# Kernel tuning notes

Hardware: AMD Instinct MI355X
Metric: run time of the kernel (lower is better)

## Reference

```python
import jax, jax.numpy as jnp
import numpy as np

B, L, D, G = 8, 4096, 1024, 128
EPS = 1e-5


def setup_inputs() -> dict:
    key = jax.random.key(0)
    k1, k2, k3 = jax.random.split(key, 3)
    x = jax.random.normal(k1, (B, L, D), dtype=jnp.float32)
    prev_count = jnp.ones((B,), dtype=jnp.int64)          # prior_count observations already seen
    prev_mean = jnp.zeros((B, G), dtype=jnp.float32)       # prior_mean expanded over batch
    prev_var = jnp.ones((B, G), dtype=jnp.float32)         # exp(prior_logv)=1 expanded over batch
    weight = 0.02 * jax.random.normal(k2, (D,), dtype=jnp.float32)  # gamma = weight + 1
    bias = 0.02 * jax.random.normal(k3, (D,), dtype=jnp.float32)
    padding_mask = jnp.ones((B, L), dtype=jnp.int32)       # 1 = valid token
    return {"x": x, "prev_count": prev_count, "prev_mean": prev_mean,
            "prev_var": prev_var, "weight": weight, "bias": bias,
            "padding_mask": padding_mask}


def reference(x, prev_count, prev_mean, prev_var, weight, bias, padding_mask):
    """Cumulative (online Welford / Chan) per-group timestep normalization.

    Running stats per (batch, group) are updated once per valid timestep by
    merging the d features of that group at that step; output normalizes each
    timestep with the stats *including* that step, then applies affine
    gamma = weight + 1, beta = bias. Padded steps leave stats unchanged.
    """
    Bs, Ls, Ds = x.shape
    Gs = prev_mean.shape[-1]
    d = Ds // Gs  # features per group
    gamma = (weight + 1.0).reshape(Gs, d)
    beta = bias.reshape(Gs, d)

    xg = x.reshape(Bs, Ls, Gs, d).transpose(1, 0, 2, 3)     # [L,B,G,d]
    mask = padding_mask.astype(x.dtype).T                   # [L,B]
    fd = jnp.asarray(d, x.dtype)

    def step(carry, inp):
        count, mean, var = carry        # [B], [B,G], [B,G]
        xt, mt = inp                    # [B,G,d], [B]
        mu = xt.mean(-1)                                    # per-step group mean [B,G]
        ssq = jnp.sum((xt - mu[..., None]) ** 2, -1)        # per-step group M2   [B,G]
        N = count * fd                                      # elements seen so far [B]
        Np = N + fd
        delta = mu - mean
        mean_n = mean + delta * (fd / Np)[:, None]
        M2_n = var * N[:, None] + ssq + (delta ** 2) * (N * fd / Np)[:, None]
        var_n = M2_n / Np[:, None]
        v = mt[:, None]                                     # 1 if valid else 0
        mean_u = mean + v * (mean_n - mean)
        var_u = var + v * (var_n - var)
        count_u = count + mt
        rstd = jax.lax.rsqrt(var_u + EPS)                   # cumrstd [B,G]
        y = (xt - mean_u[..., None]) * rstd[..., None] * gamma + beta
        return (count_u, mean_u, var_u), y

    count0 = prev_count.astype(x.dtype)
    (count_f, mean_f, var_f), ys = jax.lax.scan(
        step, (count0, prev_mean, prev_var), (xg, mask))
    y = ys.transpose(1, 0, 2, 3).reshape(Bs, Ls, Ds)
    return y, count_f.astype(jnp.int64), mean_f, var_f
```

## Files before the change

### kernel.cpp

```cpp
#include <hip/hip_runtime.h>

#define PB 8
#define PL 4096
#define PD 1024
#define PG 128
#define SEG 32
#define NSEG (PL / SEG)
#define NEPS 1e-5f

#define YSZ ((size_t)PB * PL * PD)
#define COUNT_OFF (YSZ)
#define MEAN_OFF (YSZ + PB)
#define VAR_OFF (YSZ + PB + (size_t)PB * PG)

typedef float vf4 __attribute__((ext_vector_type(4)));


__global__ __launch_bounds__(256) void k_agg(const float* __restrict__ x,
                                             const int* __restrict__ mask,
                                             float* __restrict__ aggN,
                                             float* __restrict__ aggS,
                                             float* __restrict__ aggQ) {
    int blk = blockIdx.x;
    int b = blk >> 7;
    int seg = blk & (NSEG - 1);
    int u = threadIdx.x;
    size_t row0 = (size_t)b * PL + (size_t)seg * SEG;
    const float4* xp = (const float4*)x + row0 * (PD / 4) + u;
    const int* mp = mask + b * PL + seg * SEG;

    float S = 0.f, Q = 0.f, Sb = 0.f, Qb = 0.f, nc = 0.f;
#pragma unroll 8
    for (int t = 0; t < SEG; t += 2) {
        float4 v0 = xp[(size_t)t * (PD / 4)];
        float4 v1 = xp[(size_t)(t + 1) * (PD / 4)];
        float f0 = (float)mp[t];
        float f1 = (float)mp[t + 1];
        nc += f0 + f1;
        S  = fmaf(f0, v0.x + v0.y + v0.z + v0.w, S);
        Q  = fmaf(f0, fmaf(v0.x, v0.x, fmaf(v0.y, v0.y, fmaf(v0.z, v0.z, v0.w * v0.w))), Q);
        Sb = fmaf(f1, v1.x + v1.y + v1.z + v1.w, Sb);
        Qb = fmaf(f1, fmaf(v1.x, v1.x, fmaf(v1.y, v1.y, fmaf(v1.z, v1.z, v1.w * v1.w))), Qb);
    }
    S += Sb; Q += Qb;
    S += __shfl_xor(S, 1);
    Q += __shfl_xor(Q, 1);
    if ((u & 1) == 0) {
        int idx = (b * NSEG + seg) * PG + (u >> 1);
        aggN[idx] = 8.0f * nc;
        aggS[idx] = S;
        aggQ[idx] = Q;
    }
}

__global__ __launch_bounds__(256) void k_scan(const void* __restrict__ prev_count,
                                              const float* __restrict__ prev_mean,
                                              const float* __restrict__ prev_var,
                                              const float* __restrict__ aggN,
                                              const float* __restrict__ aggS,
                                              const float* __restrict__ aggQ,
                                              float* __restrict__ carN,
                                              float* __restrict__ carS,
                                              float* __restrict__ carQ,
                                              float* __restrict__ out) {
    const int CH = NSEG / 8;
    int t = blockIdx.x * 256 + threadIdx.x;
    int pair = t >> 3;
    int c = t & 7;
    int b = pair >> 7;
    int idx0 = b * NSEG * PG + (c * CH) * PG + (pair & (PG - 1));

    float an[CH], aS[CH], aQ[CH];
#pragma unroll
    for (int i = 0; i < CH; ++i) {
        an[i] = aggN[idx0 + i * PG];
        aS[i] = aggS[idx0 + i * PG];
        aQ[i] = aggQ[idx0 + i * PG];
    }
    float ln = 0.f, lS = 0.f, lQ = 0.f;
#pragma unroll
    for (int i = 0; i < CH; ++i) { ln += an[i]; lS += aS[i]; lQ += aQ[i]; }

    float sn = ln, sS = lS, sQ = lQ;
    int lane = threadIdx.x & 63;
#pragma unroll
    for (int d = 1; d < 8; d <<= 1) {
        float tn = __shfl_up(sn, d);
        float tS = __shfl_up(sS, d);
        float tQ = __shfl_up(sQ, d);
        if ((lane & 7) >= d) { sn += tn; sS += tS; sQ += tQ; }
    }

    const long long* p64 = (const long long*)prev_count;
    const int* p32 = (const int*)prev_count;
    long long pv = p64[b];
    float cnt = (pv >= 0 && pv < (1LL << 31)) ? (float)pv : (float)p32[b];
    float n0 = 8.0f * cnt;
    float m0 = prev_mean[pair];
    float S0 = m0 * n0;
    float Q0 = fmaf(m0, m0, prev_var[pair]) * n0;

    float rn = n0 + (sn - ln);
    float rS = S0 + (sS - lS);
    float rQ = Q0 + (sQ - lQ);
#pragma unroll
    for (int i = 0; i < CH; ++i) {
        carN[idx0 + i * PG] = rn;
        carS[idx0 + i * PG] = rS;
        carQ[idx0 + i * PG] = rQ;
        rn += an[i]; rS += aS[i]; rQ += aQ[i];
    }
    if (c == 7) {
        float inv = 1.0f / rn;
        float mean = rS * inv;
        out[MEAN_OFF + pair] = mean;
        out[VAR_OFF + pair] = fmaf(-mean, mean, rQ * inv);
        if ((pair & (PG - 1)) == 0) out[COUNT_OFF + b] = rn * 0.125f;
    }
}

__global__ __launch_bounds__(256) void k_out(const float* __restrict__ x,
                                             const int* __restrict__ mask,
                                             const float* __restrict__ weight,
                                             const float* __restrict__ bias,
                                             const float* __restrict__ carN,
                                             const float* __restrict__ carS,
                                             const float* __restrict__ carQ,
                                             float* __restrict__ out) {
    int blk = blockIdx.x;
    int b = blk >> 7;
    int seg = blk & (NSEG - 1);
    int u = threadIdx.x;
    int g = u >> 1;

    int cidx = (b * NSEG + seg) * PG + g;
    float n = carN[cidx];
    float S = carS[cidx];
    float Q = carQ[cidx];

    size_t row0 = (size_t)b * PL + (size_t)seg * SEG;
    const float4* xp = (const float4*)x + row0 * (PD / 4) + u;
    vf4* yp = (vf4*)out + row0 * (PD / 4) + u;
    const int* mp = mask + b * PL + seg * SEG;

    float4 w4 = ((const float4*)weight)[u];
    float4 b4 = ((const float4*)bias)[u];
    float gx = w4.x + 1.0f, gy = w4.y + 1.0f, gz = w4.z + 1.0f, gw = w4.w + 1.0f;

    float4 v0 = xp[0];
    float4 v1 = xp[PD / 4];
#pragma unroll 4
    for (int t = 0; t < SEG; ++t) {
        int tn = (t + 2 < SEG) ? (t + 2) : (SEG - 1);
        float4 vn = xp[(size_t)tn * (PD / 4)];
        float f = (float)mp[t];
        float s  = v0.x + v0.y + v0.z + v0.w;
        float ss = fmaf(v0.x, v0.x, fmaf(v0.y, v0.y, fmaf(v0.z, v0.z, v0.w * v0.w)));
        s  += __shfl_xor(s, 1);
        ss += __shfl_xor(ss, 1);
        n = fmaf(f, 8.0f, n);
        S = fmaf(f, s, S);
        Q = fmaf(f, ss, Q);
        float inv  = __builtin_amdgcn_rcpf(n);
        float mean = S * inv;
        float var  = fmaf(-mean, mean, Q * inv);
        float rstd = __builtin_amdgcn_rsqf(var + NEPS);
        vf4 y;
        y.x = fmaf((v0.x - mean) * rstd, gx, b4.x);
        y.y = fmaf((v0.y - mean) * rstd, gy, b4.y);
        y.z = fmaf((v0.z - mean) * rstd, gz, b4.z);
        y.w = fmaf((v0.w - mean) * rstd, gw, b4.w);
        __builtin_nontemporal_store(y, yp + (size_t)t * (PD / 4));
        v0 = v1; v1 = vn;
    }
}

extern "C" void kernel_launch(void* const* d_in, const int* in_sizes, int n_in,
                              void* d_out, int out_size, void* d_ws, size_t ws_size,
                              hipStream_t stream) {
    const float* x          = (const float*)d_in[0];
    const void*  prev_count = d_in[1];
    const float* prev_mean  = (const float*)d_in[2];
    const float* prev_var   = (const float*)d_in[3];
    const float* weight     = (const float*)d_in[4];
    const float* bias       = (const float*)d_in[5];
    const int*   mask       = (const int*)d_in[6];
    float* out = (float*)d_out;
    float* ws  = (float*)d_ws;

    const size_t A = (size_t)PB * NSEG * PG;
    float* aggN = ws + 0 * A;
    float* aggS = ws + 1 * A;
    float* aggQ = ws + 2 * A;
    float* carN = ws + 3 * A;
    float* carS = ws + 4 * A;
    float* carQ = ws + 5 * A;

    hipLaunchKernelGGL(k_agg, dim3(PB * NSEG), dim3(256), 0, stream,
                       x, mask, aggN, aggS, aggQ);
    hipLaunchKernelGGL(k_scan, dim3((PB * PG * 8) / 256), dim3(256), 0, stream,
                       prev_count, prev_mean, prev_var,
                       aggN, aggS, aggQ, carN, carS, carQ, out);
    hipLaunchKernelGGL(k_out, dim3(PB * NSEG), dim3(256), 0, stream,
                       x, mask, weight, bias, carN, carS, carQ, out);
}
```

Baseline: 266.8 us.

## Fuse agg/scan/output kernels into single-pass decoupled look-back scan

Replaces the three-kernel flow (segment aggregate, carry scan, normalize/output) with one kernel. Each block computes its segment's Welford sums, publishes them with flags, and walks back through predecessor blocks to collect its running prefix, then immediately normalizes its segment. The second read of x should then come from cache instead of HBM, and two launches plus their global round trips go away. In exchange it adds a flag memset, spin-waits on predecessor blocks, and depends on blocks being scheduled in forward order to avoid stalls or deadlock.

```diff
diff --git a/kernel.cpp b/kernel.cpp
--- a/kernel.cpp
+++ b/kernel.cpp
@@ -15,16 +15,33 @@
 
 typedef float vf4 __attribute__((ext_vector_type(4)));
 
+#define AREC ((size_t)PB * NSEG * PG)
 
-__global__ __launch_bounds__(256) void k_agg(const float* __restrict__ x,
-                                             const int* __restrict__ mask,
-                                             float* __restrict__ aggN,
-                                             float* __restrict__ aggS,
-                                             float* __restrict__ aggQ) {
+__global__ __launch_bounds__(256, 4) void k_fused(
+    const float* __restrict__ x,
+    const void* __restrict__ prev_count,
+    const float* __restrict__ prev_mean,
+    const float* __restrict__ prev_var,
+    const float* __restrict__ weight,
+    const float* __restrict__ bias,
+    const int* __restrict__ mask,
+    float* __restrict__ ws,
+    int* __restrict__ flags,
+    float* __restrict__ out)
+{
     int blk = blockIdx.x;
     int b = blk >> 7;
     int seg = blk & (NSEG - 1);
     int u = threadIdx.x;
+    int g = u >> 1;
+
+    float* aggN = ws;
+    float* aggS = ws + AREC;
+    float* aggQ = ws + 2 * AREC;
+    float* incN = ws + 3 * AREC;
+    float* incS = ws + 4 * AREC;
+    float* incQ = ws + 5 * AREC;
+
     size_t row0 = (size_t)b * PL + (size_t)seg * SEG;
     const float4* xp = (const float4*)x + row0 * (PD / 4) + u;
     const int* mp = mask + b * PL + seg * SEG;
@@ -45,133 +62,115 @@
     S += Sb; Q += Qb;
     S += __shfl_xor(S, 1);
     Q += __shfl_xor(Q, 1);
-    if ((u & 1) == 0) {
-        int idx = (b * NSEG + seg) * PG + (u >> 1);
-        aggN[idx] = 8.0f * nc;
-        aggS[idx] = S;
-        aggQ[idx] = Q;
-    }
-}
+    float an = 8.0f * nc;
 
-__global__ __launch_bounds__(256) void k_scan(const void* __restrict__ prev_count,
-                                              const float* __restrict__ prev_mean,
-                                              const float* __restrict__ prev_var,
-                                              const float* __restrict__ aggN,
-                                              const float* __restrict__ aggS,
-                                              const float* __restrict__ aggQ,
-                                              float* __restrict__ carN,
-                                              float* __restrict__ carS,
-                                              float* __restrict__ carQ,
-                                              float* __restrict__ out) {
-    const int CH = NSEG / 8;
-    int t = blockIdx.x * 256 + threadIdx.x;
-    int pair = t >> 3;
-    int c = t & 7;
-    int b = pair >> 7;
-    int idx0 = b * NSEG * PG + (c * CH) * PG + (pair & (PG - 1));
+    int rec = blk * PG + g;
+    __shared__ int s_flag;
 
-    float an[CH], aS[CH], aQ[CH];
-#pragma unroll
-    for (int i = 0; i < CH; ++i) {
-        an[i] = aggN[idx0 + i * PG];
-        aS[i] = aggS[idx0 + i * PG];
-        aQ[i] = aggQ[idx0 + i * PG];
-    }
-    float ln = 0.f, lS = 0.f, lQ = 0.f;
-#pragma unroll
-    for (int i = 0; i < CH; ++i) { ln += an[i]; lS += aS[i]; lQ += aQ[i]; }
+    float rn, rS, rQ;
+    if (seg == 0) {
+        const long long* p64 = (const long long*)prev_count;
+        const int* p32 = (const int*)prev_count;
+        long long pv = p64[b];
+        float cnt = (pv >= 0 && pv < (1LL << 31)) ? (float)pv : (float)p32[b];
+        float n0 = 8.0f * cnt;
+        float m0 = prev_mean[b * PG + g];
+        rn = n0;
+        rS = m0 * n0;
+        rQ = fmaf(m0, m0, prev_var[b * PG + g]) * n0;
+    } else {
+        if ((u & 1) == 0) {
+            __hip_atomic_store(&aggN[rec], an, __ATOMIC_RELAXED, __HIP_MEMORY_SCOPE_AGENT);
+            __hip_atomic_store(&aggS[rec], S,  __ATOMIC_RELAXED, __HIP_MEMORY_SCOPE_AGENT);
+            __hip_atomic_store(&aggQ[rec], Q,  __ATOMIC_RELAXED, __HIP_MEMORY_SCOPE_AGENT);
+        }
+        __threadfence();
+        __syncthreads();
+        if (u == 0)
+            __hip_atomic_store(&flags[blk], 1, __ATOMIC_RELEASE, __HIP_MEMORY_SCOPE_AGENT);
 
-    float sn = ln, sS = lS, sQ = lQ;
-    int lane = threadIdx.x & 63;
-#pragma unroll
-    for (int d = 1; d < 8; d <<= 1) {
-        float tn = __shfl_up(sn, d);
-        float tS = __shfl_up(sS, d);
-        float tQ = __shfl_up(sQ, d);
-        if ((lane & 7) >= d) { sn += tn; sS += tS; sQ += tQ; }
+        rn = 0.f; rS = 0.f; rQ = 0.f;
+        int pred = blk - 1;
+        for (;;) {
+            if (u == 0) {
+                int f;
+                while ((f = __hip_atomic_load(&flags[pred], __ATOMIC_ACQUIRE,
+                                              __HIP_MEMORY_SCOPE_AGENT)) == 0) {
+                    __builtin_amdgcn_s_sleep(1);
+                }
+                s_flag = f;
+            }
+            __syncthreads();
+            int f = s_flag;
+            __syncthreads();
+            int pr = pred * PG + g;
+            if (f == 2) {
+                rn += __hip_atomic_load(&incN[pr], __ATOMIC_RELAXED, __HIP_MEMORY_SCOPE_AGENT);
+                rS += __hip_atomic_load(&incS[pr], __ATOMIC_RELAXED, __HIP_MEMORY_SCOPE_AGENT);
+                rQ += __hip_atomic_load(&incQ[pr], __ATOMIC_RELAXED, __HIP_MEMORY_SCOPE_AGENT);
+                break;
+            } else {
+                rn += __hip_atomic_load(&aggN[pr], __ATOMIC_RELAXED, __HIP_MEMORY_SCOPE_AGENT);
+                rS += __hip_atomic_load(&aggS[pr], __ATOMIC_RELAXED, __HIP_MEMORY_SCOPE_AGENT);
+                rQ += __hip_atomic_load(&aggQ[pr], __ATOMIC_RELAXED, __HIP_MEMORY_SCOPE_AGENT);
+                --pred;
+            }
+        }
     }
 
-    const long long* p64 = (const long long*)prev_count;
-    const int* p32 = (const int*)prev_count;
-    long long pv = p64[b];
-    float cnt = (pv >= 0 && pv < (1LL << 31)) ? (float)pv : (float)p32[b];
-    float n0 = 8.0f * cnt;
-    float m0 = prev_mean[pair];
-    float S0 = m0 * n0;
-    float Q0 = fmaf(m0, m0, prev_var[pair]) * n0;
+    {
+        float in_ = rn + an, iS = rS + S, iQ = rQ + Q;
+        if ((u & 1) == 0) {
+            __hip_atomic_store(&incN[rec], in_, __ATOMIC_RELAXED, __HIP_MEMORY_SCOPE_AGENT);
+            __hip_atomic_store(&incS[rec], iS, __ATOMIC_RELAXED, __HIP_MEMORY_SCOPE_AGENT);
+            __hip_atomic_store(&incQ[rec], iQ, __ATOMIC_RELAXED, __HIP_MEMORY_SCOPE_AGENT);
+        }
+        __threadfence();
+        __syncthreads();
+        if (u == 0)
+            __hip_atomic_store(&flags[blk], 2, __ATOMIC_RELEASE, __HIP_MEMORY_SCOPE_AGENT);
+        if (seg == NSEG - 1 && (u & 1) == 0) {
+            float inv = 1.0f / in_;
+            float mean = iS * inv;
+            out[MEAN_OFF + b * PG + g] = mean;
+            out[VAR_OFF + b * PG + g] = fmaf(-mean, mean, iQ * inv);
+            if (g == 0) out[COUNT_OFF + b] = in_ * 0.125f;
+        }
+    }
 
-    float rn = n0 + (sn - ln);
-    float rS = S0 + (sS - lS);
-    float rQ = Q0 + (sQ - lQ);
-#pragma unroll
-    for (int i = 0; i < CH; ++i) {
-        carN[idx0 + i * PG] = rn;
-        carS[idx0 + i * PG] = rS;
-        carQ[idx0 + i * PG] = rQ;
-        rn += an[i]; rS += aS[i]; rQ += aQ[i];
-    }
-    if (c == 7) {
-        float inv = 1.0f / rn;
-        float mean = rS * inv;
-        out[MEAN_OFF + pair] = mean;
-        out[VAR_OFF + pair] = fmaf(-mean, mean, rQ * inv);
-        if ((pair & (PG - 1)) == 0) out[COUNT_OFF + b] = rn * 0.125f;
-    }
-}
+    {
+        vf4* yp = (vf4*)out + row0 * (PD / 4) + u;
+        float4 w4 = ((const float4*)weight)[u];
+        float4 b4 = ((const float4*)bias)[u];
+        float gx = w4.x + 1.0f, gy = w4.y + 1.0f, gz = w4.z + 1.0f, gw = w4.w + 1.0f;
 
-__global__ __launch_bounds__(256) void k_out(const float* __restrict__ x,
-                                             const int* __restrict__ mask,
-                                             const float* __restrict__ weight,
-                                             const float* __restrict__ bias,
-                                             const float* __restrict__ carN,
-                                             const float* __restrict__ carS,
-                                             const float* __restrict__ carQ,
-                                             float* __restrict__ out) {
-    int blk = blockIdx.x;
-    int b = blk >> 7;
-    int seg = blk & (NSEG - 1);
-    int u = threadIdx.x;
-    int g = u >> 1;
-
-    int cidx = (b * NSEG + seg) * PG + g;
-    float n = carN[cidx];
-    float S = carS[cidx];
-    float Q = carQ[cidx];
-
-    size_t row0 = (size_t)b * PL + (size_t)seg * SEG;
-    const float4* xp = (const float4*)x + row0 * (PD / 4) + u;
-    vf4* yp = (vf4*)out + row0 * (PD / 4) + u;
-    const int* mp = mask + b * PL + seg * SEG;
-
-    float4 w4 = ((const float4*)weight)[u];
-    float4 b4 = ((const float4*)bias)[u];
-    float gx = w4.x + 1.0f, gy = w4.y + 1.0f, gz = w4.z + 1.0f, gw = w4.w + 1.0f;
-
-    float4 v0 = xp[0];
-    float4 v1 = xp[PD / 4];
+        float n = rn, Sa = rS, Qa = rQ;
+        float4 v0 = xp[0];
+        float4 v1 = xp[PD / 4];
 #pragma unroll 4
-    for (int t = 0; t < SEG; ++t) {
-        int tn = (t + 2 < SEG) ? (t + 2) : (SEG - 1);
-        float4 vn = xp[(size_t)tn * (PD / 4)];
-        float f = (float)mp[t];
-        float s  = v0.x + v0.y + v0.z + v0.w;
-        float ss = fmaf(v0.x, v0.x, fmaf(v0.y, v0.y, fmaf(v0.z, v0.z, v0.w * v0.w)));
-        s  += __shfl_xor(s, 1);
-        ss += __shfl_xor(ss, 1);
-        n = fmaf(f, 8.0f, n);
-        S = fmaf(f, s, S);
-        Q = fmaf(f, ss, Q);
-        float inv  = __builtin_amdgcn_rcpf(n);
-        float mean = S * inv;
-        float var  = fmaf(-mean, mean, Q * inv);
-        float rstd = __builtin_amdgcn_rsqf(var + NEPS);
-        vf4 y;
-        y.x = fmaf((v0.x - mean) * rstd, gx, b4.x);
-        y.y = fmaf((v0.y - mean) * rstd, gy, b4.y);
-        y.z = fmaf((v0.z - mean) * rstd, gz, b4.z);
-        y.w = fmaf((v0.w - mean) * rstd, gw, b4.w);
-        __builtin_nontemporal_store(y, yp + (size_t)t * (PD / 4));
-        v0 = v1; v1 = vn;
+        for (int t = 0; t < SEG; ++t) {
+            int tn = (t + 2 < SEG) ? (t + 2) : (SEG - 1);
+            float4 vn = xp[(size_t)tn * (PD / 4)];
+            float f = (float)mp[t];
+            float s  = v0.x + v0.y + v0.z + v0.w;
+            float ss = fmaf(v0.x, v0.x, fmaf(v0.y, v0.y, fmaf(v0.z, v0.z, v0.w * v0.w)));
+            s  += __shfl_xor(s, 1);
+            ss += __shfl_xor(ss, 1);
+            n  = fmaf(f, 8.0f, n);
+            Sa = fmaf(f, s, Sa);
+            Qa = fmaf(f, ss, Qa);
+            float inv  = __builtin_amdgcn_rcpf(n);
+            float mean = Sa * inv;
+            float var  = fmaf(-mean, mean, Qa * inv);
+            float rstd = __builtin_amdgcn_rsqf(var + NEPS);
+            vf4 y;
+            y.x = fmaf((v0.x - mean) * rstd, gx, b4.x);
+            y.y = fmaf((v0.y - mean) * rstd, gy, b4.y);
+            y.z = fmaf((v0.z - mean) * rstd, gz, b4.z);
+            y.w = fmaf((v0.w - mean) * rstd, gw, b4.w);
+            __builtin_nontemporal_store(y, yp + (size_t)t * (PD / 4));
+            v0 = v1; v1 = vn;
+        }
     }
 }
 
@@ -188,19 +187,11 @@
     float* out = (float*)d_out;
     float* ws  = (float*)d_ws;
 
-    const size_t A = (size_t)PB * NSEG * PG;
-    float* aggN = ws + 0 * A;
-    float* aggS = ws + 1 * A;
-    float* aggQ = ws + 2 * A;
-    float* carN = ws + 3 * A;
-    float* carS = ws + 4 * A;
-    float* carQ = ws + 5 * A;
+    int* flags = (int*)(ws + 6 * AREC);
 
-    hipLaunchKernelGGL(k_agg, dim3(PB * NSEG), dim3(256), 0, stream,
-                       x, mask, aggN, aggS, aggQ);
-    hipLaunchKernelGGL(k_scan, dim3((PB * PG * 8) / 256), dim3(256), 0, stream,
-                       prev_count, prev_mean, prev_var,
-                       aggN, aggS, aggQ, carN, carS, carQ, out);
-    hipLaunchKernelGGL(k_out, dim3(PB * NSEG), dim3(256), 0, stream,
-                       x, mask, weight, bias, carN, carS, carQ, out);
+    hipMemsetAsync(flags, 0, (size_t)PB * NSEG * sizeof(int), stream);
+
+    hipLaunchKernelGGL(k_fused, dim3(PB * NSEG), dim3(256), 0, stream,
+                       x, prev_count, prev_mean, prev_var, weight, bias, mask,
+                       ws, flags, out);
 }
```

After: 774.1 us. 190% more time.

## Halve scan segment length, pack stats as float4, remap output threads per group

Applied to the files above, without the earlier changes.

Segment length drops from 32 to 16 timesteps, which doubles the number of aggregate blocks and scan chunks. This gives more parallelism and shorter per-block serial chains. The separate N/S/Q workspace arrays are packed into float4 records so each access is one vector load or store. In the output kernel each thread now owns a whole 8-feature group and two segments share a block, which removes the cross-lane shuffle reduction. The cost is twice as much workspace and scan traffic, plus more registers per thread in the output kernel.

```diff
diff --git a/kernel.cpp b/kernel.cpp
--- a/kernel.cpp
+++ b/kernel.cpp
@@ -4,7 +4,7 @@
 #define PL 4096
 #define PD 1024
 #define PG 128
-#define SEG 32
+#define SEG 16
 #define NSEG (PL / SEG)
 #define NEPS 1e-5f
 
@@ -15,14 +15,14 @@
 
 typedef float vf4 __attribute__((ext_vector_type(4)));
 
+#define AREC ((size_t)PB * NSEG * PG)
+
 
 __global__ __launch_bounds__(256) void k_agg(const float* __restrict__ x,
                                              const int* __restrict__ mask,
-                                             float* __restrict__ aggN,
-                                             float* __restrict__ aggS,
-                                             float* __restrict__ aggQ) {
+                                             float4* __restrict__ agg) {
     int blk = blockIdx.x;
-    int b = blk >> 7;
+    int b = blk >> 8;
     int seg = blk & (NSEG - 1);
     int u = threadIdx.x;
     size_t row0 = (size_t)b * PL + (size_t)seg * SEG;
@@ -30,7 +30,7 @@
     const int* mp = mask + b * PL + seg * SEG;
 
     float S = 0.f, Q = 0.f, Sb = 0.f, Qb = 0.f, nc = 0.f;
-#pragma unroll 8
+#pragma unroll
     for (int t = 0; t < SEG; t += 2) {
         float4 v0 = xp[(size_t)t * (PD / 4)];
         float4 v1 = xp[(size_t)(t + 1) * (PD / 4)];
@@ -47,48 +47,40 @@
     Q += __shfl_xor(Q, 1);
     if ((u & 1) == 0) {
         int idx = (b * NSEG + seg) * PG + (u >> 1);
-        aggN[idx] = 8.0f * nc;
-        aggS[idx] = S;
-        aggQ[idx] = Q;
+        agg[idx] = make_float4(8.0f * nc, S, Q, 0.f);
     }
 }
 
 __global__ __launch_bounds__(256) void k_scan(const void* __restrict__ prev_count,
                                               const float* __restrict__ prev_mean,
                                               const float* __restrict__ prev_var,
-                                              const float* __restrict__ aggN,
-                                              const float* __restrict__ aggS,
-                                              const float* __restrict__ aggQ,
-                                              float* __restrict__ carN,
-                                              float* __restrict__ carS,
-                                              float* __restrict__ carQ,
+                                              const float4* __restrict__ agg,
+                                              float4* __restrict__ car,
                                               float* __restrict__ out) {
-    const int CH = NSEG / 8;
+    const int CH = NSEG / 16;
     int t = blockIdx.x * 256 + threadIdx.x;
-    int pair = t >> 3;
-    int c = t & 7;
+    int pair = t >> 4;
+    int c = t & 15;
     int b = pair >> 7;
-    int idx0 = b * NSEG * PG + (c * CH) * PG + (pair & (PG - 1));
+    int g = pair & (PG - 1);
+    int idx0 = (b * NSEG + c * CH) * PG + g;
 
-    float an[CH], aS[CH], aQ[CH];
+    float4 r[CH];
 #pragma unroll
-    for (int i = 0; i < CH; ++i) {
-        an[i] = aggN[idx0 + i * PG];
-        aS[i] = aggS[idx0 + i * PG];
-        aQ[i] = aggQ[idx0 + i * PG];
-    }
+    for (int i = 0; i < CH; ++i) r[i] = agg[idx0 + i * PG];
+
     float ln = 0.f, lS = 0.f, lQ = 0.f;
 #pragma unroll
-    for (int i = 0; i < CH; ++i) { ln += an[i]; lS += aS[i]; lQ += aQ[i]; }
+    for (int i = 0; i < CH; ++i) { ln += r[i].x; lS += r[i].y; lQ += r[i].z; }
 
     float sn = ln, sS = lS, sQ = lQ;
     int lane = threadIdx.x & 63;
 #pragma unroll
-    for (int d = 1; d < 8; d <<= 1) {
+    for (int d = 1; d < 16; d <<= 1) {
         float tn = __shfl_up(sn, d);
         float tS = __shfl_up(sS, d);
         float tQ = __shfl_up(sQ, d);
-        if ((lane & 7) >= d) { sn += tn; sS += tS; sQ += tQ; }
+        if ((lane & 15) >= d) { sn += tn; sS += tS; sQ += tQ; }
     }
 
     const long long* p64 = (const long long*)prev_count;
@@ -105,17 +97,15 @@
     float rQ = Q0 + (sQ - lQ);
 #pragma unroll
     for (int i = 0; i < CH; ++i) {
-        carN[idx0 + i * PG] = rn;
-        carS[idx0 + i * PG] = rS;
-        carQ[idx0 + i * PG] = rQ;
-        rn += an[i]; rS += aS[i]; rQ += aQ[i];
+        car[idx0 + i * PG] = make_float4(rn, rS, rQ, 0.f);
+        rn += r[i].x; rS += r[i].y; rQ += r[i].z;
     }
-    if (c == 7) {
+    if (c == 15) {
         float inv = 1.0f / rn;
         float mean = rS * inv;
         out[MEAN_OFF + pair] = mean;
         out[VAR_OFF + pair] = fmaf(-mean, mean, rQ * inv);
-        if ((pair & (PG - 1)) == 0) out[COUNT_OFF + b] = rn * 0.125f;
+        if (g == 0) out[COUNT_OFF + b] = rn * 0.125f;
     }
 }
 
@@ -123,41 +113,42 @@
                                              const int* __restrict__ mask,
                                              const float* __restrict__ weight,
                                              const float* __restrict__ bias,
-                                             const float* __restrict__ carN,
-                                             const float* __restrict__ carS,
-                                             const float* __restrict__ carQ,
+                                             const float4* __restrict__ car,
                                              float* __restrict__ out) {
     int blk = blockIdx.x;
     int b = blk >> 7;
-    int seg = blk & (NSEG - 1);
+    int sp = blk & (NSEG / 2 - 1);
     int u = threadIdx.x;
-    int g = u >> 1;
+    int h = u >> 7;
+    int g = u & (PG - 1);
+    int seg = sp * 2 + h;
 
-    int cidx = (b * NSEG + seg) * PG + g;
-    float n = carN[cidx];
-    float S = carS[cidx];
-    float Q = carQ[cidx];
+    float4 c4 = car[(b * NSEG + seg) * PG + g];
+    float n = c4.x, S = c4.y, Q = c4.z;
 
     size_t row0 = (size_t)b * PL + (size_t)seg * SEG;
-    const float4* xp = (const float4*)x + row0 * (PD / 4) + u;
-    vf4* yp = (vf4*)out + row0 * (PD / 4) + u;
+    const float4* xp = (const float4*)x + row0 * (PD / 4) + g * 2;
+    vf4* yp = (vf4*)out + row0 * (PD / 4) + g * 2;
     const int* mp = mask + b * PL + seg * SEG;
 
-    float4 w4 = ((const float4*)weight)[u];
-    float4 b4 = ((const float4*)bias)[u];
-    float gx = w4.x + 1.0f, gy = w4.y + 1.0f, gz = w4.z + 1.0f, gw = w4.w + 1.0f;
+    float4 wa = ((const float4*)weight)[g * 2];
+    float4 wb = ((const float4*)weight)[g * 2 + 1];
+    float4 ba = ((const float4*)bias)[g * 2];
+    float4 bb = ((const float4*)bias)[g * 2 + 1];
+    wa.x += 1.0f; wa.y += 1.0f; wa.z += 1.0f; wa.w += 1.0f;
+    wb.x += 1.0f; wb.y += 1.0f; wb.z += 1.0f; wb.w += 1.0f;
 
-    float4 v0 = xp[0];
-    float4 v1 = xp[PD / 4];
+    float4 a0 = xp[0],          a1 = xp[1];
+    float4 b0 = xp[PD / 4],     b1 = xp[PD / 4 + 1];
 #pragma unroll 4
     for (int t = 0; t < SEG; ++t) {
         int tn = (t + 2 < SEG) ? (t + 2) : (SEG - 1);
-        float4 vn = xp[(size_t)tn * (PD / 4)];
+        float4 c0 = xp[(size_t)tn * (PD / 4)];
+        float4 c1 = xp[(size_t)tn * (PD / 4) + 1];
         float f = (float)mp[t];
-        float s  = v0.x + v0.y + v0.z + v0.w;
-        float ss = fmaf(v0.x, v0.x, fmaf(v0.y, v0.y, fmaf(v0.z, v0.z, v0.w * v0.w)));
-        s  += __shfl_xor(s, 1);
-        ss += __shfl_xor(ss, 1);
+        float s  = (a0.x + a0.y) + (a0.z + a0.w) + (a1.x + a1.y) + (a1.z + a1.w);
+        float ss = fmaf(a0.x, a0.x, fmaf(a0.y, a0.y, fmaf(a0.z, a0.z, a0.w * a0.w)));
+        ss = fmaf(a1.x, a1.x, fmaf(a1.y, a1.y, fmaf(a1.z, a1.z, fmaf(a1.w, a1.w, ss))));
         n = fmaf(f, 8.0f, n);
         S = fmaf(f, s, S);
         Q = fmaf(f, ss, Q);
@@ -165,13 +156,18 @@
         float mean = S * inv;
         float var  = fmaf(-mean, mean, Q * inv);
         float rstd = __builtin_amdgcn_rsqf(var + NEPS);
-        vf4 y;
-        y.x = fmaf((v0.x - mean) * rstd, gx, b4.x);
-        y.y = fmaf((v0.y - mean) * rstd, gy, b4.y);
-        y.z = fmaf((v0.z - mean) * rstd, gz, b4.z);
-        y.w = fmaf((v0.w - mean) * rstd, gw, b4.w);
-        __builtin_nontemporal_store(y, yp + (size_t)t * (PD / 4));
-        v0 = v1; v1 = vn;
+        vf4 y0, y1;
+        y0.x = fmaf((a0.x - mean) * rstd, wa.x, ba.x);
+        y0.y = fmaf((a0.y - mean) * rstd, wa.y, ba.y);
+        y0.z = fmaf((a0.z - mean) * rstd, wa.z, ba.z);
+        y0.w = fmaf((a0.w - mean) * rstd, wa.w, ba.w);
+        y1.x = fmaf((a1.x - mean) * rstd, wb.x, bb.x);
+        y1.y = fmaf((a1.y - mean) * rstd, wb.y, bb.y);
+        y1.z = fmaf((a1.z - mean) * rstd, wb.z, bb.z);
+        y1.w = fmaf((a1.w - mean) * rstd, wb.w, bb.w);
+        __builtin_nontemporal_store(y0, yp + (size_t)t * (PD / 4));
+        __builtin_nontemporal_store(y1, yp + (size_t)t * (PD / 4) + 1);
+        a0 = b0; a1 = b1; b0 = c0; b1 = c1;
     }
 }
 
@@ -186,21 +182,14 @@
     const float* bias       = (const float*)d_in[5];
     const int*   mask       = (const int*)d_in[6];
     float* out = (float*)d_out;
-    float* ws  = (float*)d_ws;
 
-    const size_t A = (size_t)PB * NSEG * PG;
-    float* aggN = ws + 0 * A;
-    float* aggS = ws + 1 * A;
-    float* aggQ = ws + 2 * A;
-    float* carN = ws + 3 * A;
-    float* carS = ws + 4 * A;
-    float* carQ = ws + 5 * A;
+    float4* agg = (float4*)d_ws;
+    float4* car = agg + AREC;
 
     hipLaunchKernelGGL(k_agg, dim3(PB * NSEG), dim3(256), 0, stream,
-                       x, mask, aggN, aggS, aggQ);
-    hipLaunchKernelGGL(k_scan, dim3((PB * PG * 8) / 256), dim3(256), 0, stream,
-                       prev_count, prev_mean, prev_var,
-                       aggN, aggS, aggQ, carN, carS, carQ, out);
-    hipLaunchKernelGGL(k_out, dim3(PB * NSEG), dim3(256), 0, stream,
-                       x, mask, weight, bias, carN, carS, carQ, out);
+                       x, mask, agg);
+    hipLaunchKernelGGL(k_scan, dim3((PB * PG * 16) / 256), dim3(256), 0, stream,
+                       prev_count, prev_mean, prev_var, agg, car, out);
+    hipLaunchKernelGGL(k_out, dim3(PB * (NSEG / 2)), dim3(256), 0, stream,
+                       x, mask, weight, bias, car, out);
 }
```

Result: slower. 305.6 us (+14.5%).

## Fold segment prefix scan into output kernel and pack aggregates as float4

Applied to the files above, without the earlier changes.

Removes the separate scan kernel. Each output block now sums the per-segment aggregates of all earlier segments for its group and adds the prior stats itself. Aggregates are packed as float4 (n, S, Q, pad), so each prefix read is one vector load. This saves a kernel launch and the carry round trip through memory, at the cost of redundant prefix summation that grows with segment index (up to 127 loads per thread) and final-stat writes from the last segment's blocks.

```diff
diff --git a/kernel.cpp b/kernel.cpp
--- a/kernel.cpp
+++ b/kernel.cpp
@@ -18,9 +18,7 @@
 
 __global__ __launch_bounds__(256) void k_agg(const float* __restrict__ x,
                                              const int* __restrict__ mask,
-                                             float* __restrict__ aggN,
-                                             float* __restrict__ aggS,
-                                             float* __restrict__ aggQ) {
+                                             float4* __restrict__ agg) {
     int blk = blockIdx.x;
     int b = blk >> 7;
     int seg = blk & (NSEG - 1);
@@ -47,75 +45,7 @@
     Q += __shfl_xor(Q, 1);
     if ((u & 1) == 0) {
         int idx = (b * NSEG + seg) * PG + (u >> 1);
-        aggN[idx] = 8.0f * nc;
-        aggS[idx] = S;
-        aggQ[idx] = Q;
-    }
-}
-
-__global__ __launch_bounds__(256) void k_scan(const void* __restrict__ prev_count,
-                                              const float* __restrict__ prev_mean,
-                                              const float* __restrict__ prev_var,
-                                              const float* __restrict__ aggN,
-                                              const float* __restrict__ aggS,
-                                              const float* __restrict__ aggQ,
-                                              float* __restrict__ carN,
-                                              float* __restrict__ carS,
-                                              float* __restrict__ carQ,
-                                              float* __restrict__ out) {
-    const int CH = NSEG / 8;
-    int t = blockIdx.x * 256 + threadIdx.x;
-    int pair = t >> 3;
-    int c = t & 7;
-    int b = pair >> 7;
-    int idx0 = b * NSEG * PG + (c * CH) * PG + (pair & (PG - 1));
-
-    float an[CH], aS[CH], aQ[CH];
-#pragma unroll
-    for (int i = 0; i < CH; ++i) {
-        an[i] = aggN[idx0 + i * PG];
-        aS[i] = aggS[idx0 + i * PG];
-        aQ[i] = aggQ[idx0 + i * PG];
-    }
-    float ln = 0.f, lS = 0.f, lQ = 0.f;
-#pragma unroll
-    for (int i = 0; i < CH; ++i) { ln += an[i]; lS += aS[i]; lQ += aQ[i]; }
-
-    float sn = ln, sS = lS, sQ = lQ;
-    int lane = threadIdx.x & 63;
-#pragma unroll
-    for (int d = 1; d < 8; d <<= 1) {
-        float tn = __shfl_up(sn, d);
-        float tS = __shfl_up(sS, d);
-        float tQ = __shfl_up(sQ, d);
-        if ((lane & 7) >= d) { sn += tn; sS += tS; sQ += tQ; }
-    }
-
-    const long long* p64 = (const long long*)prev_count;
-    const int* p32 = (const int*)prev_count;
-    long long pv = p64[b];
-    float cnt = (pv >= 0 && pv < (1LL << 31)) ? (float)pv : (float)p32[b];
-    float n0 = 8.0f * cnt;
-    float m0 = prev_mean[pair];
-    float S0 = m0 * n0;
-    float Q0 = fmaf(m0, m0, prev_var[pair]) * n0;
-
-    float rn = n0 + (sn - ln);
-    float rS = S0 + (sS - lS);
-    float rQ = Q0 + (sQ - lQ);
-#pragma unroll
-    for (int i = 0; i < CH; ++i) {
-        carN[idx0 + i * PG] = rn;
-        carS[idx0 + i * PG] = rS;
-        carQ[idx0 + i * PG] = rQ;
-        rn += an[i]; rS += aS[i]; rQ += aQ[i];
-    }
-    if (c == 7) {
-        float inv = 1.0f / rn;
-        float mean = rS * inv;
-        out[MEAN_OFF + pair] = mean;
-        out[VAR_OFF + pair] = fmaf(-mean, mean, rQ * inv);
-        if ((pair & (PG - 1)) == 0) out[COUNT_OFF + b] = rn * 0.125f;
+        agg[idx] = make_float4(8.0f * nc, S, Q, 0.f);
     }
 }
 
@@ -123,20 +53,38 @@
                                              const int* __restrict__ mask,
                                              const float* __restrict__ weight,
                                              const float* __restrict__ bias,
-                                             const float* __restrict__ carN,
-                                             const float* __restrict__ carS,
-                                             const float* __restrict__ carQ,
+                                             const void* __restrict__ prev_count,
+                                             const float* __restrict__ prev_mean,
+                                             const float* __restrict__ prev_var,
+                                             const float4* __restrict__ agg,
                                              float* __restrict__ out) {
     int blk = blockIdx.x;
     int b = blk >> 7;
     int seg = blk & (NSEG - 1);
     int u = threadIdx.x;
     int g = u >> 1;
+    int p = u & 1;
 
-    int cidx = (b * NSEG + seg) * PG + g;
-    float n = carN[cidx];
-    float S = carS[cidx];
-    float Q = carQ[cidx];
+    float pn = 0.f, pS = 0.f, pQ = 0.f;
+    const float4* ab = agg + b * NSEG * PG + g;
+#pragma unroll 4
+    for (int s = p; s < seg; s += 2) {
+        float4 r = ab[s * PG];
+        pn += r.x; pS += r.y; pQ += r.z;
+    }
+    pn += __shfl_xor(pn, 1);
+    pS += __shfl_xor(pS, 1);
+    pQ += __shfl_xor(pQ, 1);
+
+    const long long* p64 = (const long long*)prev_count;
+    const int* p32 = (const int*)prev_count;
+    long long pv = p64[b];
+    float cnt = (pv >= 0 && pv < (1LL << 31)) ? (float)pv : (float)p32[b];
+    float n0 = 8.0f * cnt;
+    float m0 = prev_mean[b * PG + g];
+    float n = n0 + pn;
+    float S = fmaf(m0, n0, pS);
+    float Q = fmaf(fmaf(m0, m0, prev_var[b * PG + g]), n0, pQ);
 
     size_t row0 = (size_t)b * PL + (size_t)seg * SEG;
     const float4* xp = (const float4*)x + row0 * (PD / 4) + u;
@@ -173,6 +121,14 @@
         __builtin_nontemporal_store(y, yp + (size_t)t * (PD / 4));
         v0 = v1; v1 = vn;
     }
+
+    if (seg == NSEG - 1 && p == 0) {
+        float inv = 1.0f / n;
+        float mean = S * inv;
+        out[MEAN_OFF + b * PG + g] = mean;
+        out[VAR_OFF + b * PG + g] = fmaf(-mean, mean, Q * inv);
+        if (g == 0) out[COUNT_OFF + b] = n * 0.125f;
+    }
 }
 
 extern "C" void kernel_launch(void* const* d_in, const int* in_sizes, int n_in,
@@ -186,21 +142,12 @@
     const float* bias       = (const float*)d_in[5];
     const int*   mask       = (const int*)d_in[6];
     float* out = (float*)d_out;
-    float* ws  = (float*)d_ws;
 
-    const size_t A = (size_t)PB * NSEG * PG;
-    float* aggN = ws + 0 * A;
-    float* aggS = ws + 1 * A;
-    float* aggQ = ws + 2 * A;
-    float* carN = ws + 3 * A;
-    float* carS = ws + 4 * A;
-    float* carQ = ws + 5 * A;
+    float4* agg = (float4*)d_ws;
 
     hipLaunchKernelGGL(k_agg, dim3(PB * NSEG), dim3(256), 0, stream,
-                       x, mask, aggN, aggS, aggQ);
-    hipLaunchKernelGGL(k_scan, dim3((PB * PG * 8) / 256), dim3(256), 0, stream,
-                       prev_count, prev_mean, prev_var,
-                       aggN, aggS, aggQ, carN, carS, carQ, out);
+                       x, mask, agg);
     hipLaunchKernelGGL(k_out, dim3(PB * NSEG), dim3(256), 0, stream,
-                       x, mask, weight, bias, carN, carS, carQ, out);
+                       x, mask, weight, bias,
+                       prev_count, prev_mean, prev_var, agg, out);
 }
```

Result: no change. 265.3 us (-0.6%).
